# Optimization experiments

Hardware: AMD Instinct MI355X
Metric: run time of the kernel (lower is better)

The kernel has to match this reference:

```python
import jax, jax.numpy as jnp
import numpy as np

NUM_CHUNKS = 8
N = 8192            # points per chunk
STRIDE = 6144
TOTAL = STRIDE * (NUM_CHUNKS - 1) + N  # 51200
OVERLAP_RATIO = 0.3


def setup_inputs() -> dict:
    key = jax.random.key(0)
    ks = jax.random.split(key, 14)
    # Points in a tiny box so all pairwise distances < threshold=0.1 -> full overlap masks.
    chunks = jax.random.uniform(ks[0], (NUM_CHUNKS, N, 3), dtype=jnp.float32) * 0.05
    s = 0.1  # small conv-weight scale keeps smoothed outputs within the threshold box
    return {
        "chunks": chunks,
        "bs_w1": jax.random.normal(ks[1], (32, 3, 5), jnp.float32) * s,
        "bs_b1": jax.random.normal(ks[2], (32,), jnp.float32) * s,
        "bs_w2": jax.random.normal(ks[3], (32, 32, 5), jnp.float32) * s,
        "bs_b2": jax.random.normal(ks[4], (32,), jnp.float32) * s,
        "bs_w3": jax.random.normal(ks[5], (3, 32, 5), jnp.float32) * s,
        "bs_b3": jax.random.normal(ks[6], (3,), jnp.float32) * s,
        "wp_w1": jax.random.normal(ks[7], (32, 6, 1), jnp.float32) * s,
        "wp_b1": jax.random.normal(ks[8], (32,), jnp.float32) * s,
        "wp_w2": jax.random.normal(ks[9], (16, 32, 1), jnp.float32) * s,
        "wp_b2": jax.random.normal(ks[10], (16,), jnp.float32) * s,
        "wp_w3": jax.random.normal(ks[11], (1, 16, 1), jnp.float32) * s,
        "wp_b3": jax.random.normal(ks[12], (1,), jnp.float32) * s,
    }


def _conv1d(x, w, b, pad):
    # x: [Cin, L], w: [Cout, Cin, K] -> [Cout, L]
    y = jax.lax.conv_general_dilated(x[None], w, (1,), [(pad, pad)],
                                     dimension_numbers=("NCH", "OIH", "NCH"))[0]
    return y + b[:, None]


def reference(chunks, bs_w1, bs_b1, bs_w2, bs_b2, bs_w3, bs_b3,
              wp_w1, wp_b1, wp_w2, wp_b2, wp_w3, wp_b3):
    def boundary_smoother(x):   # x: [3, L] -> [3, L]
        h = jax.nn.relu(_conv1d(x, bs_w1, bs_b1, 2))
        h = jax.nn.relu(_conv1d(h, bs_w2, bs_b2, 2))
        return _conv1d(h, bs_w3, bs_b3, 2)

    def weight_predictor(x):    # x: [6, L] -> [L]
        h = jax.nn.relu(_conv1d(x, wp_w1, wp_b1, 0))
        h = jax.nn.relu(_conv1d(h, wp_w2, wp_b2, 0))
        return jax.nn.sigmoid(_conv1d(h, wp_w3, wp_b3, 0))[0]

    def smooth_pair(p, c):      # p, c: [N, 3]; full overlap (masks all-True by construction)
        # squared cdist via the Gram trick; argmin equals cdist argmin
        d2 = (jnp.sum(p * p, 1)[:, None] + jnp.sum(c * c, 1)[None, :]
              - 2.0 * p @ c.T)                       # [N, N]
        mi = jnp.argmin(d2, axis=1)                  # [N]
        matched = c[mi]                              # [N, 3]
        feat = jnp.concatenate([p.T, matched.T], 0)  # [6, N]
        w = weight_predictor(feat)                   # [N]
        fused = w[:, None] * p + (1.0 - w)[:, None] * matched
        sm = boundary_smoother(fused.T).T            # [N, 3]
        # chunk1 fully overlapped -> replaced; chunk2 scatter-written at matched idx
        return sm, c.at[mi].set(sm)

    smoothed = [chunks[0]]
    for i in range(1, NUM_CHUNKS):
        p_new, c_new = smooth_pair(smoothed[-1], chunks[i])
        smoothed[-1] = p_new
        smoothed.append(c_new)
    stacked = jnp.stack(smoothed)                    # [C, N, 3]

    # fade-weighted scatter-add merge
    fade = int(N * OVERLAP_RATIO / 2)
    cw = jnp.ones(N, jnp.float32)
    cw = cw.at[:fade].set(jnp.linspace(0.1, 1.0, fade, dtype=jnp.float32))
    cw = cw.at[-fade:].set(jnp.linspace(1.0, 0.1, fade, dtype=jnp.float32))
    idx = (np.arange(NUM_CHUNKS)[:, None] * STRIDE + np.arange(N)).reshape(-1)
    merged = jnp.zeros((TOTAL, 3), jnp.float32).at[idx].add(
        (stacked * cw[None, :, None]).reshape(-1, 3))
    wsum = jnp.zeros(TOTAL, jnp.float32).at[idx].add(
        jnp.broadcast_to(cw, (NUM_CHUNKS, N)).reshape(-1))
    return merged / jnp.maximum(wsum, 1e-8)[:, None]
```

## Files before the change

### kernel.cpp

```cpp
#include <hip/hip_runtime.h>

#define NPTS 8192
#define NCH 8
#define STRIDE 6144
#define TOTAL 51200
#define FADE 1228
#define SEG 32
#define SEGLEN 256
#define JB 4
#define TEAMS 4
#define TLEN 64

__global__ void k_setup(const float* __restrict__ chunks, float* __restrict__ fin,
                        int* __restrict__ jmax_all, unsigned int* __restrict__ packed32) {
    int i = blockIdx.x * 256 + threadIdx.x;
    if (i < NCH * NPTS * 3) fin[i] = chunks[i];
    if (i < (NCH - 1) * NPTS) jmax_all[i] = -1;
    if (i < (NCH - 1) * NPTS * 2) packed32[i] = 0xFFFFFFFFu;
}

__global__ __launch_bounds__(1024) void k_argmin(const float* __restrict__ P,
                                                 const float* __restrict__ C,
                                                 unsigned long long* __restrict__ packed) {
#pragma clang fp contract(off)
    __shared__ float4 sh[SEGLEN];
    __shared__ unsigned long long pkbuf[TEAMS - 1][1024];
    int tid = threadIdx.x;
    int lt   = tid & 255;
    int team = tid >> 8;
    int k0 = blockIdx.y * SEGLEN;
    if (tid < SEGLEN) {
        int k = k0 + tid;
        float x = C[k * 3 + 0], y = C[k * 3 + 1], z = C[k * 3 + 2];
        float cc = (x * x + y * y) + z * z;
        sh[tid] = make_float4(x, y, z, cc);
    }
    __syncthreads();
    int j0 = blockIdx.x * (256 * JB) + lt * JB;
    const float4* Pv = (const float4*)(P + j0 * 3);
    float4 a = Pv[0], b = Pv[1], c4 = Pv[2];
    float p0[JB] = {a.x, a.w, b.z, c4.y};
    float p1[JB] = {a.y, b.x, b.w, c4.z};
    float p2[JB] = {a.z, b.y, c4.x, c4.w};
    float pp[JB], best[JB];
    int bt[JB];
    int t0 = team * TLEN;
#pragma unroll
    for (int i = 0; i < JB; ++i) {
        pp[i] = (p0[i] * p0[i] + p1[i] * p1[i]) + p2[i] * p2[i];
        best[i] = 3.4e38f;
        bt[i] = t0;
    }
#pragma unroll 4
    for (int tt = 0; tt < TLEN; ++tt) {
        int t = t0 + tt;
        float4 f = sh[t];
#pragma unroll
        for (int i = 0; i < JB; ++i) {
            float g = __builtin_fmaf(p2[i], f.z, __builtin_fmaf(p1[i], f.y, p0[i] * f.x));
            float sadd = pp[i] + f.w;
            float d = __builtin_fmaf(-2.0f, g, sadd);
            if (d < best[i]) { best[i] = d; bt[i] = t; }
        }
    }
    unsigned long long pk[JB];
#pragma unroll
    for (int i = 0; i < JB; ++i) {
        unsigned ud = __float_as_uint(best[i]);
        if (ud == 0x80000000u) ud = 0u;
        ud = (ud & 0x80000000u) ? ~ud : (ud | 0x80000000u);
        pk[i] = ((unsigned long long)ud << 32)
              | (unsigned long long)(unsigned)(k0 + bt[i]);
    }
    if (team > 0) {
#pragma unroll
        for (int i = 0; i < JB; ++i) pkbuf[team - 1][lt * JB + i] = pk[i];
    }
    __syncthreads();
    if (team == 0) {
#pragma unroll
        for (int i = 0; i < JB; ++i) {
            unsigned long long v = pk[i];
            unsigned long long v1 = pkbuf[0][lt * JB + i];
            unsigned long long v2 = pkbuf[1][lt * JB + i];
            unsigned long long v3 = pkbuf[2][lt * JB + i];
            if (v1 < v) v = v1;
            if (v2 < v) v = v2;
            if (v3 < v) v = v3;
            atomicMin(&packed[j0 + i], v);
        }
    }
}

__global__ __launch_bounds__(128) void k_resolve(
        const float* __restrict__ P, const float* __restrict__ C,
        const unsigned long long* __restrict__ packed,
        const float* __restrict__ w1g, const float* __restrict__ b1g,
        const float* __restrict__ w2g, const float* __restrict__ b2g,
        const float* __restrict__ w3g, const float* __restrict__ b3g,
        float* __restrict__ fused, int* __restrict__ mi, int* __restrict__ jmax) {
#pragma clang fp contract(off)
    __shared__ float W[780];
    int tid = threadIdx.x;
    for (int i = tid; i < 780; i += 128) {
        float v;
        if (i < 192) v = w1g[i];
        else if (i < 224) v = b1g[i - 192];
        else if (i < 736) v = w2g[i - 224];
        else if (i < 752) v = b2g[i - 736];
        else if (i < 768) v = w3g[i - 752];
        else v = b3g[0];
        W[i] = v;
    }
    __syncthreads();

    int j = blockIdx.x * 128 + tid;
    int m = (int)(unsigned)(packed[j] & 0xFFFFFFFFull);
    mi[j] = m;
    float x6[6];
    x6[0] = P[j * 3 + 0]; x6[1] = P[j * 3 + 1]; x6[2] = P[j * 3 + 2];
    x6[3] = C[m * 3 + 0]; x6[4] = C[m * 3 + 1]; x6[5] = C[m * 3 + 2];

    float h1[32];
#pragma unroll
    for (int o = 0; o < 32; ++o) {
        float acc = 0.0f;
#pragma unroll
        for (int ci = 0; ci < 6; ++ci) acc = __builtin_fmaf(x6[ci], W[o * 6 + ci], acc);
        h1[o] = fmaxf(acc + W[192 + o], 0.0f);
    }
    float h2[16];
#pragma unroll
    for (int o = 0; o < 16; ++o) {
        float acc = 0.0f;
#pragma unroll
        for (int ci = 0; ci < 32; ++ci) acc = __builtin_fmaf(h1[ci], W[224 + o * 32 + ci], acc);
        h2[o] = fmaxf(acc + W[736 + o], 0.0f);
    }
    float acc = 0.0f;
#pragma unroll
    for (int ci = 0; ci < 16; ++ci) acc = __builtin_fmaf(h2[ci], W[752 + ci], acc);
    float z = acc + W[768];
    float w = 1.0f / (1.0f + expf(-z));
    float omw = 1.0f - w;
#pragma unroll
    for (int e = 0; e < 3; ++e) {
        float t1 = w * x6[e];
        float t2 = omw * x6[3 + e];
        fused[e * NPTS + j] = t1 + t2;
    }

    int lane = tid & 63;
    bool issue = true;
    for (int s = 1; s < 64; ++s) {
        int om = __shfl_down(m, s);
        if (lane + s < 64 && om == m) issue = false;
    }
    if (issue) atomicMax(&jmax[m], j);
}

#define S1 41
#define S2 37
__global__ __launch_bounds__(256) void k_smoother(const float* __restrict__ fused,
        const float* __restrict__ w1g, const float* __restrict__ b1g,
        const float* __restrict__ w2g, const float* __restrict__ b2g,
        const float* __restrict__ w3g, const float* __restrict__ b3g,
        float* __restrict__ sm, const int* __restrict__ mi,
        const int* __restrict__ jmax, float* __restrict__ finNext) {
#pragma clang fp contract(off)
    __shared__ float F[3][44];
    __shared__ float H1[32][S1];
    __shared__ float H2[32][S2];
    __shared__ float W2[5120];
    __shared__ float B2[32];
    int tid = threadIdx.x;
    int BASE = blockIdx.x * 32;

    for (int li = tid; li < 132; li += 256) {
        int c = li / 44, i = li % 44;
        int t = BASE - 6 + i;
        F[c][i] = (t >= 0 && t < NPTS) ? fused[c * NPTS + t] : 0.0f;
    }
    for (int li = tid; li < 1280; li += 256) {
        float4 v = ((const float4*)w2g)[li];
        int base = li * 4;
#pragma unroll
        for (int u = 0; u < 4; ++u) {
            int idx = base + u;
            int co = idx / 160;
            int r = idx - co * 160;
            int ci = r / 5;
            int k = r - ci * 5;
            W2[(ci * 5 + k) * 32 + co] = (&v.x)[u];
        }
    }
    if (tid < 32) B2[tid] = b2g[tid];
    __syncthreads();

    {
        int co = tid >> 3, pg = tid & 7;
        float wr[15];
#pragma unroll
        for (int q = 0; q < 15; ++q) wr[q] = w1g[co * 15 + q];
        float bias = b1g[co];
#pragma unroll
        for (int s = 0; s < 5; ++s) {
            int i = pg * 5 + s;
            int t = BASE - 4 + i;
            float acc = 0.0f;
#pragma unroll
            for (int k = 0; k < 5; ++k)
#pragma unroll
                for (int ci = 0; ci < 3; ++ci)
                    acc = __builtin_fmaf(F[ci][i + k], wr[ci * 5 + k], acc);
            H1[co][i] = (t >= 0 && t < NPTS) ? fmaxf(acc + bias, 0.0f) : 0.0f;
        }
    }
    __syncthreads();

    {
        int cq = tid & 7, pp = tid >> 3;
        if (pp < 18) {
            int i2 = pp * 2;
            int co0 = cq * 4;
            float acc00 = 0.f, acc01 = 0.f, acc02 = 0.f, acc03 = 0.f;
            float acc10 = 0.f, acc11 = 0.f, acc12 = 0.f, acc13 = 0.f;
            for (int k = 0; k < 5; ++k) {
#pragma unroll
                for (int ci = 0; ci < 32; ++ci) {
                    float in0 = H1[ci][i2 + k];
                    float in1 = H1[ci][i2 + k + 1];
                    const float4 wv = *(const float4*)&W2[(ci * 5 + k) * 32 + co0];
                    acc00 = __builtin_fmaf(in0, wv.x, acc00);
                    acc01 = __builtin_fmaf(in0, wv.y, acc01);
                    acc02 = __builtin_fmaf(in0, wv.z, acc02);
                    acc03 = __builtin_fmaf(in0, wv.w, acc03);
                    acc10 = __builtin_fmaf(in1, wv.x, acc10);
                    acc11 = __builtin_fmaf(in1, wv.y, acc11);
                    acc12 = __builtin_fmaf(in1, wv.z, acc12);
                    acc13 = __builtin_fmaf(in1, wv.w, acc13);
                }
            }
            int t0 = BASE - 2 + i2, t1 = t0 + 1;
            bool ok0 = (t0 >= 0 && t0 < NPTS), ok1 = (t1 >= 0 && t1 < NPTS);
            H2[co0 + 0][i2]     = ok0 ? fmaxf(acc00 + B2[co0 + 0], 0.0f) : 0.0f;
            H2[co0 + 1][i2]     = ok0 ? fmaxf(acc01 + B2[co0 + 1], 0.0f) : 0.0f;
            H2[co0 + 2][i2]     = ok0 ? fmaxf(acc02 + B2[co0 + 2], 0.0f) : 0.0f;
            H2[co0 + 3][i2]     = ok0 ? fmaxf(acc03 + B2[co0 + 3], 0.0f) : 0.0f;
            H2[co0 + 0][i2 + 1] = ok1 ? fmaxf(acc10 + B2[co0 + 0], 0.0f) : 0.0f;
            H2[co0 + 1][i2 + 1] = ok1 ? fmaxf(acc11 + B2[co0 + 1], 0.0f) : 0.0f;
            H2[co0 + 2][i2 + 1] = ok1 ? fmaxf(acc12 + B2[co0 + 2], 0.0f) : 0.0f;
            H2[co0 + 3][i2 + 1] = ok1 ? fmaxf(acc13 + B2[co0 + 3], 0.0f) : 0.0f;
        }
    }
    __syncthreads();

    if (tid < 96) {
        int co = tid >> 5, p = tid & 31;
        float wr[160];
        const float4* w3v = (const float4*)(w3g + co * 160);
#pragma unroll
        for (int q = 0; q < 40; ++q) {
            float4 v = w3v[q];
            wr[q * 4 + 0] = v.x; wr[q * 4 + 1] = v.y;
            wr[q * 4 + 2] = v.z; wr[q * 4 + 3] = v.w;
        }
        float acc = 0.0f;
#pragma unroll
        for (int k = 0; k < 5; ++k)
#pragma unroll
            for (int ci = 0; ci < 32; ++ci)
                acc = __builtin_fmaf(H2[ci][p + k], wr[ci * 5 + k], acc);
        float val = acc + b3g[co];
        int jj = BASE + p;
        sm[jj * 3 + co] = val;
        int kk = mi[jj];
        if (jmax[kk] == jj) finNext[kk * 3 + co] = val;
    }
}

__global__ void k_merge(const float* __restrict__ fin, float* __restrict__ out) {
#pragma clang fp contract(off)
    int pos = blockIdx.x * 256 + threadIdx.x;
    if (pos >= TOTAL) return;
    int imax = pos / STRIDE; if (imax > NCH - 1) imax = NCH - 1;
    int imin = (pos >= NPTS) ? ((pos - NPTS) / STRIDE + 1) : 0;
    float a0 = 0.0f, a1 = 0.0f, a2 = 0.0f, wsum = 0.0f;
    const float kstep = 0.9f / 1227.0f;
    for (int i = imin; i <= imax; ++i) {
        int t = pos - i * STRIDE;
        float cw;
        if (t < FADE)                cw = 0.1f + (float)t * kstep;
        else if (t >= NPTS - FADE)   cw = 1.0f - (float)(t - (NPTS - FADE)) * kstep;
        else                         cw = 1.0f;
        const float* v = fin + (i * NPTS + t) * 3;
        a0 += cw * v[0];
        a1 += cw * v[1];
        a2 += cw * v[2];
        wsum += cw;
    }
    float wm = fmaxf(wsum, 1e-8f);
    out[pos * 3 + 0] = a0 / wm;
    out[pos * 3 + 1] = a1 / wm;
    out[pos * 3 + 2] = a2 / wm;
}

extern "C" void kernel_launch(void* const* d_in, const int* in_sizes, int n_in,
                              void* d_out, int out_size, void* d_ws, size_t ws_size,
                              hipStream_t stream) {
    const float* chunks = (const float*)d_in[0];
    const float* bs_w1 = (const float*)d_in[1];
    const float* bs_b1 = (const float*)d_in[2];
    const float* bs_w2 = (const float*)d_in[3];
    const float* bs_b2 = (const float*)d_in[4];
    const float* bs_w3 = (const float*)d_in[5];
    const float* bs_b3 = (const float*)d_in[6];
    const float* wp_w1 = (const float*)d_in[7];
    const float* wp_b1 = (const float*)d_in[8];
    const float* wp_w2 = (const float*)d_in[9];
    const float* wp_b2 = (const float*)d_in[10];
    const float* wp_w3 = (const float*)d_in[11];
    const float* wp_b3 = (const float*)d_in[12];

    unsigned long long* packed_all = (unsigned long long*)d_ws;
    float* fin      = (float*)(packed_all + (NCH - 1) * NPTS);
    float* fused    = fin + NCH * NPTS * 3;
    int*   mi       = (int*)(fused + 3 * NPTS);
    int*   jmax_all = mi + NPTS;

    k_setup<<<768, 256, 0, stream>>>(chunks, fin, jmax_all, (unsigned int*)packed_all);

    for (int i = 1; i < NCH; ++i) {
        const float* C = chunks + i * NPTS * 3;
        float* P  = fin + (i - 1) * NPTS * 3;
        float* Pn = fin + i * NPTS * 3;
        unsigned long long* packed = packed_all + (i - 1) * NPTS;
        int* jmax = jmax_all + (i - 1) * NPTS;

        k_argmin<<<dim3(NPTS / (256 * JB), SEG), 1024, 0, stream>>>(P, C, packed);
        k_resolve<<<64, 128, 0, stream>>>(P, C, packed, wp_w1, wp_b1, wp_w2, wp_b2,
                                          wp_w3, wp_b3, fused, mi, jmax);
        k_smoother<<<256, 256, 0, stream>>>(fused, bs_w1, bs_b1, bs_w2, bs_b2,
                                            bs_w3, bs_b3, P, mi, jmax, Pn);
    }

    k_merge<<<200, 256, 0, stream>>>(fin, (float*)d_out);
}
```

Baseline: 328.4 us.

## Fuse all per-chunk kernels into one cooperative persistent kernel with grid syncs

Replaces the setup, 7×(argmin, resolve, smoother), and merge launches with a single cooperative kernel of 256 blocks × 1024 threads that uses grid.sync between phases. Weights are staged into shared memory once and reused across iterations, and the wave-level dedup before atomicMax is dropped. This removes about 23 kernel launches and their gaps. In exchange, the resolve and smoother phases run on only 32–256 threads of each 1024-thread block, and grid-wide barriers add their own cost. The launch also requires all 256 blocks to be co-resident.

```diff
diff --git a/kernel.cpp b/kernel.cpp
--- a/kernel.cpp
+++ b/kernel.cpp
@@ -1,4 +1,7 @@
 #include <hip/hip_runtime.h>
+#include <hip/hip_cooperative_groups.h>
+
+namespace cg = cooperative_groups;
 
 #define NPTS 8192
 #define NCH 8
@@ -10,179 +13,62 @@
 #define JB 4
 #define TEAMS 4
 #define TLEN 64
-
-__global__ void k_setup(const float* __restrict__ chunks, float* __restrict__ fin,
-                        int* __restrict__ jmax_all, unsigned int* __restrict__ packed32) {
-    int i = blockIdx.x * 256 + threadIdx.x;
-    if (i < NCH * NPTS * 3) fin[i] = chunks[i];
-    if (i < (NCH - 1) * NPTS) jmax_all[i] = -1;
-    if (i < (NCH - 1) * NPTS * 2) packed32[i] = 0xFFFFFFFFu;
-}
-
-__global__ __launch_bounds__(1024) void k_argmin(const float* __restrict__ P,
-                                                 const float* __restrict__ C,
-                                                 unsigned long long* __restrict__ packed) {
+#define S1 41
+#define S2 37
+
+__global__ __launch_bounds__(1024, 4) void k_mega(
+        const float* __restrict__ chunks,
+        const float* __restrict__ bs_w1, const float* __restrict__ bs_b1,
+        const float* __restrict__ bs_w2, const float* __restrict__ bs_b2,
+        const float* __restrict__ bs_w3, const float* __restrict__ bs_b3,
+        const float* __restrict__ wp_w1, const float* __restrict__ wp_b1,
+        const float* __restrict__ wp_w2, const float* __restrict__ wp_b2,
+        const float* __restrict__ wp_w3, const float* __restrict__ wp_b3,
+        float* __restrict__ out, unsigned long long* ws) {
 #pragma clang fp contract(off)
+    cg::grid_group grid = cg::this_grid();
+
     __shared__ float4 sh[SEGLEN];
     __shared__ unsigned long long pkbuf[TEAMS - 1][1024];
-    int tid = threadIdx.x;
-    int lt   = tid & 255;
-    int team = tid >> 8;
-    int k0 = blockIdx.y * SEGLEN;
-    if (tid < SEGLEN) {
-        int k = k0 + tid;
-        float x = C[k * 3 + 0], y = C[k * 3 + 1], z = C[k * 3 + 2];
-        float cc = (x * x + y * y) + z * z;
-        sh[tid] = make_float4(x, y, z, cc);
-    }
-    __syncthreads();
-    int j0 = blockIdx.x * (256 * JB) + lt * JB;
-    const float4* Pv = (const float4*)(P + j0 * 3);
-    float4 a = Pv[0], b = Pv[1], c4 = Pv[2];
-    float p0[JB] = {a.x, a.w, b.z, c4.y};
-    float p1[JB] = {a.y, b.x, b.w, c4.z};
-    float p2[JB] = {a.z, b.y, c4.x, c4.w};
-    float pp[JB], best[JB];
-    int bt[JB];
-    int t0 = team * TLEN;
-#pragma unroll
-    for (int i = 0; i < JB; ++i) {
-        pp[i] = (p0[i] * p0[i] + p1[i] * p1[i]) + p2[i] * p2[i];
-        best[i] = 3.4e38f;
-        bt[i] = t0;
-    }
-#pragma unroll 4
-    for (int tt = 0; tt < TLEN; ++tt) {
-        int t = t0 + tt;
-        float4 f = sh[t];
-#pragma unroll
-        for (int i = 0; i < JB; ++i) {
-            float g = __builtin_fmaf(p2[i], f.z, __builtin_fmaf(p1[i], f.y, p0[i] * f.x));
-            float sadd = pp[i] + f.w;
-            float d = __builtin_fmaf(-2.0f, g, sadd);
-            if (d < best[i]) { best[i] = d; bt[i] = t; }
-        }
-    }
-    unsigned long long pk[JB];
-#pragma unroll
-    for (int i = 0; i < JB; ++i) {
-        unsigned ud = __float_as_uint(best[i]);
-        if (ud == 0x80000000u) ud = 0u;
-        ud = (ud & 0x80000000u) ? ~ud : (ud | 0x80000000u);
-        pk[i] = ((unsigned long long)ud << 32)
-              | (unsigned long long)(unsigned)(k0 + bt[i]);
-    }
-    if (team > 0) {
-#pragma unroll
-        for (int i = 0; i < JB; ++i) pkbuf[team - 1][lt * JB + i] = pk[i];
-    }
-    __syncthreads();
-    if (team == 0) {
-#pragma unroll
-        for (int i = 0; i < JB; ++i) {
-            unsigned long long v = pk[i];
-            unsigned long long v1 = pkbuf[0][lt * JB + i];
-            unsigned long long v2 = pkbuf[1][lt * JB + i];
-            unsigned long long v3 = pkbuf[2][lt * JB + i];
-            if (v1 < v) v = v1;
-            if (v2 < v) v = v2;
-            if (v3 < v) v = v3;
-            atomicMin(&packed[j0 + i], v);
-        }
-    }
-}
-
-__global__ __launch_bounds__(128) void k_resolve(
-        const float* __restrict__ P, const float* __restrict__ C,
-        const unsigned long long* __restrict__ packed,
-        const float* __restrict__ w1g, const float* __restrict__ b1g,
-        const float* __restrict__ w2g, const float* __restrict__ b2g,
-        const float* __restrict__ w3g, const float* __restrict__ b3g,
-        float* __restrict__ fused, int* __restrict__ mi, int* __restrict__ jmax) {
-#pragma clang fp contract(off)
-    __shared__ float W[780];
-    int tid = threadIdx.x;
-    for (int i = tid; i < 780; i += 128) {
-        float v;
-        if (i < 192) v = w1g[i];
-        else if (i < 224) v = b1g[i - 192];
-        else if (i < 736) v = w2g[i - 224];
-        else if (i < 752) v = b2g[i - 736];
-        else if (i < 768) v = w3g[i - 752];
-        else v = b3g[0];
-        W[i] = v;
-    }
-    __syncthreads();
-
-    int j = blockIdx.x * 128 + tid;
-    int m = (int)(unsigned)(packed[j] & 0xFFFFFFFFull);
-    mi[j] = m;
-    float x6[6];
-    x6[0] = P[j * 3 + 0]; x6[1] = P[j * 3 + 1]; x6[2] = P[j * 3 + 2];
-    x6[3] = C[m * 3 + 0]; x6[4] = C[m * 3 + 1]; x6[5] = C[m * 3 + 2];
-
-    float h1[32];
-#pragma unroll
-    for (int o = 0; o < 32; ++o) {
-        float acc = 0.0f;
-#pragma unroll
-        for (int ci = 0; ci < 6; ++ci) acc = __builtin_fmaf(x6[ci], W[o * 6 + ci], acc);
-        h1[o] = fmaxf(acc + W[192 + o], 0.0f);
-    }
-    float h2[16];
-#pragma unroll
-    for (int o = 0; o < 16; ++o) {
-        float acc = 0.0f;
-#pragma unroll
-        for (int ci = 0; ci < 32; ++ci) acc = __builtin_fmaf(h1[ci], W[224 + o * 32 + ci], acc);
-        h2[o] = fmaxf(acc + W[736 + o], 0.0f);
-    }
-    float acc = 0.0f;
-#pragma unroll
-    for (int ci = 0; ci < 16; ++ci) acc = __builtin_fmaf(h2[ci], W[752 + ci], acc);
-    float z = acc + W[768];
-    float w = 1.0f / (1.0f + expf(-z));
-    float omw = 1.0f - w;
-#pragma unroll
-    for (int e = 0; e < 3; ++e) {
-        float t1 = w * x6[e];
-        float t2 = omw * x6[3 + e];
-        fused[e * NPTS + j] = t1 + t2;
-    }
-
-    int lane = tid & 63;
-    bool issue = true;
-    for (int s = 1; s < 64; ++s) {
-        int om = __shfl_down(m, s);
-        if (lane + s < 64 && om == m) issue = false;
-    }
-    if (issue) atomicMax(&jmax[m], j);
-}
-
-#define S1 41
-#define S2 37
-__global__ __launch_bounds__(256) void k_smoother(const float* __restrict__ fused,
-        const float* __restrict__ w1g, const float* __restrict__ b1g,
-        const float* __restrict__ w2g, const float* __restrict__ b2g,
-        const float* __restrict__ w3g, const float* __restrict__ b3g,
-        float* __restrict__ sm, const int* __restrict__ mi,
-        const int* __restrict__ jmax, float* __restrict__ finNext) {
-#pragma clang fp contract(off)
+    __shared__ float Wp[780];
     __shared__ float F[3][44];
     __shared__ float H1[32][S1];
     __shared__ float H2[32][S2];
+    __shared__ float W1s[480];
+    __shared__ float B1s[32];
     __shared__ float W2[5120];
     __shared__ float B2[32];
+    __shared__ float W3s[480];
+    __shared__ float B3s[3];
+
+    unsigned long long* packed_all = ws;
+    float* fin      = (float*)(packed_all + (NCH - 1) * NPTS);
+    float* fused    = fin + NCH * NPTS * 3;
+    int*   mi       = (int*)(fused + 3 * NPTS);
+    int*   jmax_all = mi + NPTS;
+
     int tid = threadIdx.x;
-    int BASE = blockIdx.x * 32;
-
-    for (int li = tid; li < 132; li += 256) {
-        int c = li / 44, i = li % 44;
-        int t = BASE - 6 + i;
-        F[c][i] = (t >= 0 && t < NPTS) ? fused[c * NPTS + t] : 0.0f;
-    }
-    for (int li = tid; li < 1280; li += 256) {
-        float4 v = ((const float4*)w2g)[li];
+    int bid = blockIdx.x;
+    int gtid = bid * 1024 + tid;
+
+    if (gtid < NCH * NPTS * 3) fin[gtid] = chunks[gtid];
+    if (gtid < (NCH - 1) * NPTS) {
+        jmax_all[gtid] = -1;
+        packed_all[gtid] = 0xFFFFFFFFFFFFFFFFull;
+    }
+
+    for (int i = tid; i < 780; i += 1024) {
+        float v;
+        if (i < 192) v = wp_w1[i];
+        else if (i < 224) v = wp_b1[i - 192];
+        else if (i < 736) v = wp_w2[i - 224];
+        else if (i < 752) v = wp_b2[i - 736];
+        else if (i < 768) v = wp_w3[i - 752];
+        else v = wp_b3[0];
+        Wp[i] = v;
+    }
+    for (int li = tid; li < 1280; li += 1024) {
+        float4 v = ((const float4*)bs_w2)[li];
         int base = li * 4;
 #pragma unroll
         for (int u = 0; u < 4; ++u) {
@@ -194,115 +80,235 @@
             W2[(ci * 5 + k) * 32 + co] = (&v.x)[u];
         }
     }
-    if (tid < 32) B2[tid] = b2g[tid];
-    __syncthreads();
-
-    {
-        int co = tid >> 3, pg = tid & 7;
-        float wr[15];
-#pragma unroll
-        for (int q = 0; q < 15; ++q) wr[q] = w1g[co * 15 + q];
-        float bias = b1g[co];
-#pragma unroll
-        for (int s = 0; s < 5; ++s) {
-            int i = pg * 5 + s;
-            int t = BASE - 4 + i;
+    for (int i = tid; i < 480; i += 1024) { W1s[i] = bs_w1[i]; W3s[i] = bs_w3[i]; }
+    if (tid < 32) { B1s[tid] = bs_b1[tid]; B2[tid] = bs_b2[tid]; }
+    if (tid < 3)  B3s[tid] = bs_b3[tid];
+
+    grid.sync();
+
+    for (int it = 1; it < NCH; ++it) {
+        const float* C = chunks + it * NPTS * 3;
+        float* P  = fin + (it - 1) * NPTS * 3;
+        float* Pn = fin + it * NPTS * 3;
+        unsigned long long* packed = packed_all + (it - 1) * NPTS;
+        int* jmax = jmax_all + (it - 1) * NPTS;
+
+        {
+            int bx = bid & 7, by = bid >> 3;
+            int lt = tid & 255, team = tid >> 8;
+            int k0 = by * SEGLEN;
+            if (tid < SEGLEN) {
+                int k = k0 + tid;
+                float x = C[k * 3 + 0], y = C[k * 3 + 1], z = C[k * 3 + 2];
+                float cc = (x * x + y * y) + z * z;
+                sh[tid] = make_float4(x, y, z, cc);
+            }
+            __syncthreads();
+            int j0 = bx * (256 * JB) + lt * JB;
+            const float4* Pv = (const float4*)(P + j0 * 3);
+            float4 a = Pv[0], b = Pv[1], c4 = Pv[2];
+            float p0[JB] = {a.x, a.w, b.z, c4.y};
+            float p1[JB] = {a.y, b.x, b.w, c4.z};
+            float p2[JB] = {a.z, b.y, c4.x, c4.w};
+            float pp[JB], best[JB];
+            int bt[JB];
+            int t0 = team * TLEN;
+#pragma unroll
+            for (int i = 0; i < JB; ++i) {
+                pp[i] = (p0[i] * p0[i] + p1[i] * p1[i]) + p2[i] * p2[i];
+                best[i] = 3.4e38f;
+                bt[i] = t0;
+            }
+#pragma unroll 4
+            for (int tt = 0; tt < TLEN; ++tt) {
+                int t = t0 + tt;
+                float4 f = sh[t];
+#pragma unroll
+                for (int i = 0; i < JB; ++i) {
+                    float g = __builtin_fmaf(p2[i], f.z, __builtin_fmaf(p1[i], f.y, p0[i] * f.x));
+                    float sadd = pp[i] + f.w;
+                    float d = __builtin_fmaf(-2.0f, g, sadd);
+                    if (d < best[i]) { best[i] = d; bt[i] = t; }
+                }
+            }
+            unsigned long long pk[JB];
+#pragma unroll
+            for (int i = 0; i < JB; ++i) {
+                unsigned ud = __float_as_uint(best[i]);
+                if (ud == 0x80000000u) ud = 0u;
+                ud = (ud & 0x80000000u) ? ~ud : (ud | 0x80000000u);
+                pk[i] = ((unsigned long long)ud << 32)
+                      | (unsigned long long)(unsigned)(k0 + bt[i]);
+            }
+            if (team > 0) {
+#pragma unroll
+                for (int i = 0; i < JB; ++i) pkbuf[team - 1][lt * JB + i] = pk[i];
+            }
+            __syncthreads();
+            if (team == 0) {
+#pragma unroll
+                for (int i = 0; i < JB; ++i) {
+                    unsigned long long v = pk[i];
+                    unsigned long long v1 = pkbuf[0][lt * JB + i];
+                    unsigned long long v2 = pkbuf[1][lt * JB + i];
+                    unsigned long long v3 = pkbuf[2][lt * JB + i];
+                    if (v1 < v) v = v1;
+                    if (v2 < v) v = v2;
+                    if (v3 < v) v = v3;
+                    atomicMin(&packed[j0 + i], v);
+                }
+            }
+        }
+        grid.sync();
+
+        if (tid < 32) {
+            int j = bid * 32 + tid;
+            int m = (int)(unsigned)(packed[j] & 0xFFFFFFFFull);
+            mi[j] = m;
+            float x6[6];
+            x6[0] = P[j * 3 + 0]; x6[1] = P[j * 3 + 1]; x6[2] = P[j * 3 + 2];
+            x6[3] = C[m * 3 + 0]; x6[4] = C[m * 3 + 1]; x6[5] = C[m * 3 + 2];
+
+            float h1[32];
+#pragma unroll
+            for (int o = 0; o < 32; ++o) {
+                float acc = 0.0f;
+#pragma unroll
+                for (int ci = 0; ci < 6; ++ci) acc = __builtin_fmaf(x6[ci], Wp[o * 6 + ci], acc);
+                h1[o] = fmaxf(acc + Wp[192 + o], 0.0f);
+            }
+            float h2[16];
+#pragma unroll
+            for (int o = 0; o < 16; ++o) {
+                float acc = 0.0f;
+#pragma unroll
+                for (int ci = 0; ci < 32; ++ci) acc = __builtin_fmaf(h1[ci], Wp[224 + o * 32 + ci], acc);
+                h2[o] = fmaxf(acc + Wp[736 + o], 0.0f);
+            }
             float acc = 0.0f;
 #pragma unroll
-            for (int k = 0; k < 5; ++k)
-#pragma unroll
-                for (int ci = 0; ci < 3; ++ci)
-                    acc = __builtin_fmaf(F[ci][i + k], wr[ci * 5 + k], acc);
-            H1[co][i] = (t >= 0 && t < NPTS) ? fmaxf(acc + bias, 0.0f) : 0.0f;
-        }
-    }
-    __syncthreads();
-
-    {
-        int cq = tid & 7, pp = tid >> 3;
-        if (pp < 18) {
-            int i2 = pp * 2;
-            int co0 = cq * 4;
-            float acc00 = 0.f, acc01 = 0.f, acc02 = 0.f, acc03 = 0.f;
-            float acc10 = 0.f, acc11 = 0.f, acc12 = 0.f, acc13 = 0.f;
-            for (int k = 0; k < 5; ++k) {
-#pragma unroll
-                for (int ci = 0; ci < 32; ++ci) {
-                    float in0 = H1[ci][i2 + k];
-                    float in1 = H1[ci][i2 + k + 1];
-                    const float4 wv = *(const float4*)&W2[(ci * 5 + k) * 32 + co0];
-                    acc00 = __builtin_fmaf(in0, wv.x, acc00);
-                    acc01 = __builtin_fmaf(in0, wv.y, acc01);
-                    acc02 = __builtin_fmaf(in0, wv.z, acc02);
-                    acc03 = __builtin_fmaf(in0, wv.w, acc03);
-                    acc10 = __builtin_fmaf(in1, wv.x, acc10);
-                    acc11 = __builtin_fmaf(in1, wv.y, acc11);
-                    acc12 = __builtin_fmaf(in1, wv.z, acc12);
-                    acc13 = __builtin_fmaf(in1, wv.w, acc13);
+            for (int ci = 0; ci < 16; ++ci) acc = __builtin_fmaf(h2[ci], Wp[752 + ci], acc);
+            float z = acc + Wp[768];
+            float w = 1.0f / (1.0f + expf(-z));
+            float omw = 1.0f - w;
+#pragma unroll
+            for (int e = 0; e < 3; ++e) {
+                float t1 = w * x6[e];
+                float t2 = omw * x6[3 + e];
+                fused[e * NPTS + j] = t1 + t2;
+            }
+            atomicMax(&jmax[m], j);
+        }
+        grid.sync();
+
+        {
+            int BASE = bid * 32;
+            for (int li = tid; li < 132; li += 1024) {
+                int c = li / 44, i = li % 44;
+                int t = BASE - 6 + i;
+                F[c][i] = (t >= 0 && t < NPTS) ? fused[c * NPTS + t] : 0.0f;
+            }
+            __syncthreads();
+
+            if (tid < 256) {
+                int co = tid >> 3, pg = tid & 7;
+                float wr[15];
+#pragma unroll
+                for (int q = 0; q < 15; ++q) wr[q] = W1s[co * 15 + q];
+                float bias = B1s[co];
+#pragma unroll
+                for (int s = 0; s < 5; ++s) {
+                    int i = pg * 5 + s;
+                    int t = BASE - 4 + i;
+                    float acc = 0.0f;
+#pragma unroll
+                    for (int k = 0; k < 5; ++k)
+#pragma unroll
+                        for (int ci = 0; ci < 3; ++ci)
+                            acc = __builtin_fmaf(F[ci][i + k], wr[ci * 5 + k], acc);
+                    H1[co][i] = (t >= 0 && t < NPTS) ? fmaxf(acc + bias, 0.0f) : 0.0f;
                 }
             }
-            int t0 = BASE - 2 + i2, t1 = t0 + 1;
-            bool ok0 = (t0 >= 0 && t0 < NPTS), ok1 = (t1 >= 0 && t1 < NPTS);
-            H2[co0 + 0][i2]     = ok0 ? fmaxf(acc00 + B2[co0 + 0], 0.0f) : 0.0f;
-            H2[co0 + 1][i2]     = ok0 ? fmaxf(acc01 + B2[co0 + 1], 0.0f) : 0.0f;
-            H2[co0 + 2][i2]     = ok0 ? fmaxf(acc02 + B2[co0 + 2], 0.0f) : 0.0f;
-            H2[co0 + 3][i2]     = ok0 ? fmaxf(acc03 + B2[co0 + 3], 0.0f) : 0.0f;
-            H2[co0 + 0][i2 + 1] = ok1 ? fmaxf(acc10 + B2[co0 + 0], 0.0f) : 0.0f;
-            H2[co0 + 1][i2 + 1] = ok1 ? fmaxf(acc11 + B2[co0 + 1], 0.0f) : 0.0f;
-            H2[co0 + 2][i2 + 1] = ok1 ? fmaxf(acc12 + B2[co0 + 2], 0.0f) : 0.0f;
-            H2[co0 + 3][i2 + 1] = ok1 ? fmaxf(acc13 + B2[co0 + 3], 0.0f) : 0.0f;
-        }
-    }
-    __syncthreads();
-
-    if (tid < 96) {
-        int co = tid >> 5, p = tid & 31;
-        float wr[160];
-        const float4* w3v = (const float4*)(w3g + co * 160);
-#pragma unroll
-        for (int q = 0; q < 40; ++q) {
-            float4 v = w3v[q];
-            wr[q * 4 + 0] = v.x; wr[q * 4 + 1] = v.y;
-            wr[q * 4 + 2] = v.z; wr[q * 4 + 3] = v.w;
-        }
-        float acc = 0.0f;
-#pragma unroll
-        for (int k = 0; k < 5; ++k)
-#pragma unroll
-            for (int ci = 0; ci < 32; ++ci)
-                acc = __builtin_fmaf(H2[ci][p + k], wr[ci * 5 + k], acc);
-        float val = acc + b3g[co];
-        int jj = BASE + p;
-        sm[jj * 3 + co] = val;
-        int kk = mi[jj];
-        if (jmax[kk] == jj) finNext[kk * 3 + co] = val;
-    }
-}
-
-__global__ void k_merge(const float* __restrict__ fin, float* __restrict__ out) {
-#pragma clang fp contract(off)
-    int pos = blockIdx.x * 256 + threadIdx.x;
-    if (pos >= TOTAL) return;
-    int imax = pos / STRIDE; if (imax > NCH - 1) imax = NCH - 1;
-    int imin = (pos >= NPTS) ? ((pos - NPTS) / STRIDE + 1) : 0;
-    float a0 = 0.0f, a1 = 0.0f, a2 = 0.0f, wsum = 0.0f;
-    const float kstep = 0.9f / 1227.0f;
-    for (int i = imin; i <= imax; ++i) {
-        int t = pos - i * STRIDE;
-        float cw;
-        if (t < FADE)                cw = 0.1f + (float)t * kstep;
-        else if (t >= NPTS - FADE)   cw = 1.0f - (float)(t - (NPTS - FADE)) * kstep;
-        else                         cw = 1.0f;
-        const float* v = fin + (i * NPTS + t) * 3;
-        a0 += cw * v[0];
-        a1 += cw * v[1];
-        a2 += cw * v[2];
-        wsum += cw;
-    }
-    float wm = fmaxf(wsum, 1e-8f);
-    out[pos * 3 + 0] = a0 / wm;
-    out[pos * 3 + 1] = a1 / wm;
-    out[pos * 3 + 2] = a2 / wm;
+            __syncthreads();
+
+            {
+                int cq = tid & 7, pq = tid >> 3;
+                if (pq < 18) {
+                    int i2 = pq * 2;
+                    int co0 = cq * 4;
+                    float acc00 = 0.f, acc01 = 0.f, acc02 = 0.f, acc03 = 0.f;
+                    float acc10 = 0.f, acc11 = 0.f, acc12 = 0.f, acc13 = 0.f;
+                    for (int k = 0; k < 5; ++k) {
+#pragma unroll
+                        for (int ci = 0; ci < 32; ++ci) {
+                            float in0 = H1[ci][i2 + k];
+                            float in1 = H1[ci][i2 + k + 1];
+                            const float4 wv = *(const float4*)&W2[(ci * 5 + k) * 32 + co0];
+                            acc00 = __builtin_fmaf(in0, wv.x, acc00);
+                            acc01 = __builtin_fmaf(in0, wv.y, acc01);
+                            acc02 = __builtin_fmaf(in0, wv.z, acc02);
+                            acc03 = __builtin_fmaf(in0, wv.w, acc03);
+                            acc10 = __builtin_fmaf(in1, wv.x, acc10);
+                            acc11 = __builtin_fmaf(in1, wv.y, acc11);
+                            acc12 = __builtin_fmaf(in1, wv.z, acc12);
+                            acc13 = __builtin_fmaf(in1, wv.w, acc13);
+                        }
+                    }
+                    int t0 = BASE - 2 + i2, t1 = t0 + 1;
+                    bool ok0 = (t0 >= 0 && t0 < NPTS), ok1 = (t1 >= 0 && t1 < NPTS);
+                    H2[co0 + 0][i2]     = ok0 ? fmaxf(acc00 + B2[co0 + 0], 0.0f) : 0.0f;
+                    H2[co0 + 1][i2]     = ok0 ? fmaxf(acc01 + B2[co0 + 1], 0.0f) : 0.0f;
+                    H2[co0 + 2][i2]     = ok0 ? fmaxf(acc02 + B2[co0 + 2], 0.0f) : 0.0f;
+                    H2[co0 + 3][i2]     = ok0 ? fmaxf(acc03 + B2[co0 + 3], 0.0f) : 0.0f;
+                    H2[co0 + 0][i2 + 1] = ok1 ? fmaxf(acc10 + B2[co0 + 0], 0.0f) : 0.0f;
+                    H2[co0 + 1][i2 + 1] = ok1 ? fmaxf(acc11 + B2[co0 + 1], 0.0f) : 0.0f;
+                    H2[co0 + 2][i2 + 1] = ok1 ? fmaxf(acc12 + B2[co0 + 2], 0.0f) : 0.0f;
+                    H2[co0 + 3][i2 + 1] = ok1 ? fmaxf(acc13 + B2[co0 + 3], 0.0f) : 0.0f;
+                }
+            }
+            __syncthreads();
+
+            if (tid < 96) {
+                int co = tid >> 5, p = tid & 31;
+                float acc = 0.0f;
+#pragma unroll
+                for (int k = 0; k < 5; ++k)
+#pragma unroll
+                    for (int ci = 0; ci < 32; ++ci)
+                        acc = __builtin_fmaf(H2[ci][p + k], W3s[co * 160 + ci * 5 + k], acc);
+                float val = acc + B3s[co];
+                int jj = BASE + p;
+                P[jj * 3 + co] = val;
+                int kk = mi[jj];
+                if (jmax[kk] == jj) Pn[kk * 3 + co] = val;
+            }
+        }
+        grid.sync();
+    }
+
+    if (gtid < TOTAL) {
+        int pos = gtid;
+        int imax = pos / STRIDE; if (imax > NCH - 1) imax = NCH - 1;
+        int imin = (pos >= NPTS) ? ((pos - NPTS) / STRIDE + 1) : 0;
+        float a0 = 0.0f, a1 = 0.0f, a2 = 0.0f, wsum = 0.0f;
+        const float kstep = 0.9f / 1227.0f;
+        for (int i = imin; i <= imax; ++i) {
+            int t = pos - i * STRIDE;
+            float cw;
+            if (t < FADE)                cw = 0.1f + (float)t * kstep;
+            else if (t >= NPTS - FADE)   cw = 1.0f - (float)(t - (NPTS - FADE)) * kstep;
+            else                         cw = 1.0f;
+            const float* v = fin + (i * NPTS + t) * 3;
+            a0 += cw * v[0];
+            a1 += cw * v[1];
+            a2 += cw * v[2];
+            wsum += cw;
+        }
+        float wm = fmaxf(wsum, 1e-8f);
+        out[pos * 3 + 0] = a0 / wm;
+        out[pos * 3 + 1] = a1 / wm;
+        out[pos * 3 + 2] = a2 / wm;
+    }
 }
 
 extern "C" void kernel_launch(void* const* d_in, const int* in_sizes, int n_in,
@@ -321,28 +327,16 @@
     const float* wp_b2 = (const float*)d_in[10];
     const float* wp_w3 = (const float*)d_in[11];
     const float* wp_b3 = (const float*)d_in[12];
-
-    unsigned long long* packed_all = (unsigned long long*)d_ws;
-    float* fin      = (float*)(packed_all + (NCH - 1) * NPTS);
-    float* fused    = fin + NCH * NPTS * 3;
-    int*   mi       = (int*)(fused + 3 * NPTS);
-    int*   jmax_all = mi + NPTS;
-
-    k_setup<<<768, 256, 0, stream>>>(chunks, fin, jmax_all, (unsigned int*)packed_all);
-
-    for (int i = 1; i < NCH; ++i) {
-        const float* C = chunks + i * NPTS * 3;
-        float* P  = fin + (i - 1) * NPTS * 3;
-        float* Pn = fin + i * NPTS * 3;
-        unsigned long long* packed = packed_all + (i - 1) * NPTS;
-        int* jmax = jmax_all + (i - 1) * NPTS;
-
-        k_argmin<<<dim3(NPTS / (256 * JB), SEG), 1024, 0, stream>>>(P, C, packed);
-        k_resolve<<<64, 128, 0, stream>>>(P, C, packed, wp_w1, wp_b1, wp_w2, wp_b2,
-                                          wp_w3, wp_b3, fused, mi, jmax);
-        k_smoother<<<256, 256, 0, stream>>>(fused, bs_w1, bs_b1, bs_w2, bs_b2,
-                                            bs_w3, bs_b3, P, mi, jmax, Pn);
-    }
-
-    k_merge<<<200, 256, 0, stream>>>(fin, (float*)d_out);
+    float* outp = (float*)d_out;
+    unsigned long long* wsp = (unsigned long long*)d_ws;
+
+    void* args[] = {
+        (void*)&chunks,
+        (void*)&bs_w1, (void*)&bs_b1, (void*)&bs_w2, (void*)&bs_b2,
+        (void*)&bs_w3, (void*)&bs_b3,
+        (void*)&wp_w1, (void*)&wp_b1, (void*)&wp_w2, (void*)&wp_b2,
+        (void*)&wp_w3, (void*)&wp_b3,
+        (void*)&outp, (void*)&wsp};
+    hipLaunchCooperativeKernel((const void*)k_mega, dim3(256), dim3(1024),
+                               args, 0, stream);
 }
```

After: 1.017 ms. 210% more time.

## Fuse resolve into smoother and replace jmax pass with packed 64-bit atomicMax scatter

Applied to the files above, without the earlier changes.

Merges the weight-predictor kernel into the smoother kernel, so each block computes its own fused inputs (a 32-point tile plus a 12-point halo) in shared memory. This removes one launch per chunk pair and the global round trip of the fused, mi and jmax arrays. The last-writer scatter rule is now a single 64-bit atomicMax that packs (index+1, value) into 64-bit point storage, which replaces the separate jmax resolution. In exchange, halo points are recomputed redundantly and point loads in argmin and merge become 64-bit reads at twice the bandwidth. Only 44 threads per block run the MLP, which serializes that phase.

```diff
diff --git a/kernel.cpp b/kernel.cpp
--- a/kernel.cpp
+++ b/kernel.cpp
@@ -10,21 +10,24 @@
 #define JB 4
 #define TEAMS 4
 #define TLEN 64
-
-__global__ void k_setup(const float* __restrict__ chunks, float* __restrict__ fin,
-                        int* __restrict__ jmax_all, unsigned int* __restrict__ packed32) {
+#define S1 41
+#define S2 37
+
+typedef unsigned long long u64;
+
+__global__ void k_setup(const float* __restrict__ chunks, u64* __restrict__ PK,
+                        u64* __restrict__ packed_all) {
     int i = blockIdx.x * 256 + threadIdx.x;
-    if (i < NCH * NPTS * 3) fin[i] = chunks[i];
-    if (i < (NCH - 1) * NPTS) jmax_all[i] = -1;
-    if (i < (NCH - 1) * NPTS * 2) packed32[i] = 0xFFFFFFFFu;
-}
-
-__global__ __launch_bounds__(1024) void k_argmin(const float* __restrict__ P,
+    if (i < NCH * NPTS * 3) PK[i] = (u64)__float_as_uint(chunks[i]);
+    if (i < (NCH - 1) * NPTS) packed_all[i] = 0xFFFFFFFFFFFFFFFFull;
+}
+
+__global__ __launch_bounds__(1024) void k_argmin(const u64* __restrict__ PKprev,
                                                  const float* __restrict__ C,
-                                                 unsigned long long* __restrict__ packed) {
+                                                 u64* __restrict__ packed) {
 #pragma clang fp contract(off)
     __shared__ float4 sh[SEGLEN];
-    __shared__ unsigned long long pkbuf[TEAMS - 1][1024];
+    __shared__ u64 pkbuf[TEAMS - 1][1024];
     int tid = threadIdx.x;
     int lt   = tid & 255;
     int team = tid >> 8;
@@ -37,11 +40,13 @@
     }
     __syncthreads();
     int j0 = blockIdx.x * (256 * JB) + lt * JB;
-    const float4* Pv = (const float4*)(P + j0 * 3);
-    float4 a = Pv[0], b = Pv[1], c4 = Pv[2];
-    float p0[JB] = {a.x, a.w, b.z, c4.y};
-    float p1[JB] = {a.y, b.x, b.w, c4.z};
-    float p2[JB] = {a.z, b.y, c4.x, c4.w};
+    const u64* Pq = PKprev + (size_t)j0 * 3;
+    float p[12];
+#pragma unroll
+    for (int n = 0; n < 12; ++n) p[n] = __uint_as_float((unsigned)Pq[n]);
+    float p0[JB] = {p[0], p[3], p[6], p[9]};
+    float p1[JB] = {p[1], p[4], p[7], p[10]};
+    float p2[JB] = {p[2], p[5], p[8], p[11]};
     float pp[JB], best[JB];
     int bt[JB];
     int t0 = team * TLEN;
@@ -63,14 +68,13 @@
             if (d < best[i]) { best[i] = d; bt[i] = t; }
         }
     }
-    unsigned long long pk[JB];
+    u64 pk[JB];
 #pragma unroll
     for (int i = 0; i < JB; ++i) {
         unsigned ud = __float_as_uint(best[i]);
         if (ud == 0x80000000u) ud = 0u;
         ud = (ud & 0x80000000u) ? ~ud : (ud | 0x80000000u);
-        pk[i] = ((unsigned long long)ud << 32)
-              | (unsigned long long)(unsigned)(k0 + bt[i]);
+        pk[i] = ((u64)ud << 32) | (u64)(unsigned)(k0 + bt[i]);
     }
     if (team > 0) {
 #pragma unroll
@@ -80,10 +84,10 @@
     if (team == 0) {
 #pragma unroll
         for (int i = 0; i < JB; ++i) {
-            unsigned long long v = pk[i];
-            unsigned long long v1 = pkbuf[0][lt * JB + i];
-            unsigned long long v2 = pkbuf[1][lt * JB + i];
-            unsigned long long v3 = pkbuf[2][lt * JB + i];
+            u64 v = pk[i];
+            u64 v1 = pkbuf[0][lt * JB + i];
+            u64 v2 = pkbuf[1][lt * JB + i];
+            u64 v3 = pkbuf[2][lt * JB + i];
             if (v1 < v) v = v1;
             if (v2 < v) v = v2;
             if (v3 < v) v = v3;
@@ -92,83 +96,20 @@
     }
 }
 
-__global__ __launch_bounds__(128) void k_resolve(
-        const float* __restrict__ P, const float* __restrict__ C,
-        const unsigned long long* __restrict__ packed,
+__global__ __launch_bounds__(256) void k_rsm(
+        const u64* __restrict__ PKprev, const float* __restrict__ C,
+        const u64* __restrict__ packed,
+        const float* __restrict__ wp_w1, const float* __restrict__ wp_b1,
+        const float* __restrict__ wp_w2, const float* __restrict__ wp_b2,
+        const float* __restrict__ wp_w3, const float* __restrict__ wp_b3,
         const float* __restrict__ w1g, const float* __restrict__ b1g,
         const float* __restrict__ w2g, const float* __restrict__ b2g,
         const float* __restrict__ w3g, const float* __restrict__ b3g,
-        float* __restrict__ fused, int* __restrict__ mi, int* __restrict__ jmax) {
+        float* __restrict__ finOut, u64* __restrict__ PKnext) {
 #pragma clang fp contract(off)
-    __shared__ float W[780];
-    int tid = threadIdx.x;
-    for (int i = tid; i < 780; i += 128) {
-        float v;
-        if (i < 192) v = w1g[i];
-        else if (i < 224) v = b1g[i - 192];
-        else if (i < 736) v = w2g[i - 224];
-        else if (i < 752) v = b2g[i - 736];
-        else if (i < 768) v = w3g[i - 752];
-        else v = b3g[0];
-        W[i] = v;
-    }
-    __syncthreads();
-
-    int j = blockIdx.x * 128 + tid;
-    int m = (int)(unsigned)(packed[j] & 0xFFFFFFFFull);
-    mi[j] = m;
-    float x6[6];
-    x6[0] = P[j * 3 + 0]; x6[1] = P[j * 3 + 1]; x6[2] = P[j * 3 + 2];
-    x6[3] = C[m * 3 + 0]; x6[4] = C[m * 3 + 1]; x6[5] = C[m * 3 + 2];
-
-    float h1[32];
-#pragma unroll
-    for (int o = 0; o < 32; ++o) {
-        float acc = 0.0f;
-#pragma unroll
-        for (int ci = 0; ci < 6; ++ci) acc = __builtin_fmaf(x6[ci], W[o * 6 + ci], acc);
-        h1[o] = fmaxf(acc + W[192 + o], 0.0f);
-    }
-    float h2[16];
-#pragma unroll
-    for (int o = 0; o < 16; ++o) {
-        float acc = 0.0f;
-#pragma unroll
-        for (int ci = 0; ci < 32; ++ci) acc = __builtin_fmaf(h1[ci], W[224 + o * 32 + ci], acc);
-        h2[o] = fmaxf(acc + W[736 + o], 0.0f);
-    }
-    float acc = 0.0f;
-#pragma unroll
-    for (int ci = 0; ci < 16; ++ci) acc = __builtin_fmaf(h2[ci], W[752 + ci], acc);
-    float z = acc + W[768];
-    float w = 1.0f / (1.0f + expf(-z));
-    float omw = 1.0f - w;
-#pragma unroll
-    for (int e = 0; e < 3; ++e) {
-        float t1 = w * x6[e];
-        float t2 = omw * x6[3 + e];
-        fused[e * NPTS + j] = t1 + t2;
-    }
-
-    int lane = tid & 63;
-    bool issue = true;
-    for (int s = 1; s < 64; ++s) {
-        int om = __shfl_down(m, s);
-        if (lane + s < 64 && om == m) issue = false;
-    }
-    if (issue) atomicMax(&jmax[m], j);
-}
-
-#define S1 41
-#define S2 37
-__global__ __launch_bounds__(256) void k_smoother(const float* __restrict__ fused,
-        const float* __restrict__ w1g, const float* __restrict__ b1g,
-        const float* __restrict__ w2g, const float* __restrict__ b2g,
-        const float* __restrict__ w3g, const float* __restrict__ b3g,
-        float* __restrict__ sm, const int* __restrict__ mi,
-        const int* __restrict__ jmax, float* __restrict__ finNext) {
-#pragma clang fp contract(off)
+    __shared__ float Wp[780];
     __shared__ float F[3][44];
+    __shared__ int   MIs[44];
     __shared__ float H1[32][S1];
     __shared__ float H2[32][S2];
     __shared__ float W2[5120];
@@ -176,10 +117,15 @@
     int tid = threadIdx.x;
     int BASE = blockIdx.x * 32;
 
-    for (int li = tid; li < 132; li += 256) {
-        int c = li / 44, i = li % 44;
-        int t = BASE - 6 + i;
-        F[c][i] = (t >= 0 && t < NPTS) ? fused[c * NPTS + t] : 0.0f;
+    for (int i = tid; i < 780; i += 256) {
+        float v;
+        if (i < 192) v = wp_w1[i];
+        else if (i < 224) v = wp_b1[i - 192];
+        else if (i < 736) v = wp_w2[i - 224];
+        else if (i < 752) v = wp_b2[i - 736];
+        else if (i < 768) v = wp_w3[i - 752];
+        else v = wp_b3[0];
+        Wp[i] = v;
     }
     for (int li = tid; li < 1280; li += 256) {
         float4 v = ((const float4*)w2g)[li];
@@ -197,6 +143,52 @@
     if (tid < 32) B2[tid] = b2g[tid];
     __syncthreads();
 
+    if (tid < 44) {
+        int jt = BASE - 6 + tid;
+        if (jt >= 0 && jt < NPTS) {
+            int m = (int)(unsigned)(packed[jt] & 0xFFFFFFFFull);
+            MIs[tid] = m;
+            float x6[6];
+            x6[0] = __uint_as_float((unsigned)PKprev[(size_t)jt * 3 + 0]);
+            x6[1] = __uint_as_float((unsigned)PKprev[(size_t)jt * 3 + 1]);
+            x6[2] = __uint_as_float((unsigned)PKprev[(size_t)jt * 3 + 2]);
+            x6[3] = C[m * 3 + 0]; x6[4] = C[m * 3 + 1]; x6[5] = C[m * 3 + 2];
+
+            float h1[32];
+#pragma unroll
+            for (int o = 0; o < 32; ++o) {
+                float acc = 0.0f;
+#pragma unroll
+                for (int ci = 0; ci < 6; ++ci) acc = __builtin_fmaf(x6[ci], Wp[o * 6 + ci], acc);
+                h1[o] = fmaxf(acc + Wp[192 + o], 0.0f);
+            }
+            float h2[16];
+#pragma unroll
+            for (int o = 0; o < 16; ++o) {
+                float acc = 0.0f;
+#pragma unroll
+                for (int ci = 0; ci < 32; ++ci) acc = __builtin_fmaf(h1[ci], Wp[224 + o * 32 + ci], acc);
+                h2[o] = fmaxf(acc + Wp[736 + o], 0.0f);
+            }
+            float acc = 0.0f;
+#pragma unroll
+            for (int ci = 0; ci < 16; ++ci) acc = __builtin_fmaf(h2[ci], Wp[752 + ci], acc);
+            float z = acc + Wp[768];
+            float w = 1.0f / (1.0f + expf(-z));
+            float omw = 1.0f - w;
+#pragma unroll
+            for (int e = 0; e < 3; ++e) {
+                float t1 = w * x6[e];
+                float t2 = omw * x6[3 + e];
+                F[e][tid] = t1 + t2;
+            }
+        } else {
+            F[0][tid] = 0.0f; F[1][tid] = 0.0f; F[2][tid] = 0.0f;
+            MIs[tid] = 0;
+        }
+    }
+    __syncthreads();
+
     {
         int co = tid >> 3, pg = tid & 7;
         float wr[15];
@@ -219,9 +211,9 @@
     __syncthreads();
 
     {
-        int cq = tid & 7, pp = tid >> 3;
-        if (pp < 18) {
-            int i2 = pp * 2;
+        int cq = tid & 7, pq = tid >> 3;
+        if (pq < 18) {
+            int i2 = pq * 2;
             int co0 = cq * 4;
             float acc00 = 0.f, acc01 = 0.f, acc02 = 0.f, acc03 = 0.f;
             float acc10 = 0.f, acc11 = 0.f, acc12 = 0.f, acc13 = 0.f;
@@ -273,13 +265,15 @@
                 acc = __builtin_fmaf(H2[ci][p + k], wr[ci * 5 + k], acc);
         float val = acc + b3g[co];
         int jj = BASE + p;
-        sm[jj * 3 + co] = val;
-        int kk = mi[jj];
-        if (jmax[kk] == jj) finNext[kk * 3 + co] = val;
-    }
-}
-
-__global__ void k_merge(const float* __restrict__ fin, float* __restrict__ out) {
+        finOut[jj * 3 + co] = val;
+        int kk = MIs[p + 6];
+        atomicMax(&PKnext[(size_t)kk * 3 + co],
+                  ((u64)(unsigned)(jj + 1) << 32) | (u64)__float_as_uint(val));
+    }
+}
+
+__global__ void k_merge(const float* __restrict__ fin, const u64* __restrict__ PK7,
+                        float* __restrict__ out) {
 #pragma clang fp contract(off)
     int pos = blockIdx.x * 256 + threadIdx.x;
     if (pos >= TOTAL) return;
@@ -293,10 +287,19 @@
         if (t < FADE)                cw = 0.1f + (float)t * kstep;
         else if (t >= NPTS - FADE)   cw = 1.0f - (float)(t - (NPTS - FADE)) * kstep;
         else                         cw = 1.0f;
-        const float* v = fin + (i * NPTS + t) * 3;
-        a0 += cw * v[0];
-        a1 += cw * v[1];
-        a2 += cw * v[2];
+        float v0, v1, v2;
+        if (i < NCH - 1) {
+            const float* v = fin + ((size_t)i * NPTS + t) * 3;
+            v0 = v[0]; v1 = v[1]; v2 = v[2];
+        } else {
+            const u64* q = PK7 + (size_t)t * 3;
+            v0 = __uint_as_float((unsigned)q[0]);
+            v1 = __uint_as_float((unsigned)q[1]);
+            v2 = __uint_as_float((unsigned)q[2]);
+        }
+        a0 += cw * v0;
+        a1 += cw * v1;
+        a2 += cw * v2;
         wsum += cw;
     }
     float wm = fmaxf(wsum, 1e-8f);
@@ -322,27 +325,25 @@
     const float* wp_w3 = (const float*)d_in[11];
     const float* wp_b3 = (const float*)d_in[12];
 
-    unsigned long long* packed_all = (unsigned long long*)d_ws;
-    float* fin      = (float*)(packed_all + (NCH - 1) * NPTS);
-    float* fused    = fin + NCH * NPTS * 3;
-    int*   mi       = (int*)(fused + 3 * NPTS);
-    int*   jmax_all = mi + NPTS;
-
-    k_setup<<<768, 256, 0, stream>>>(chunks, fin, jmax_all, (unsigned int*)packed_all);
-
-    for (int i = 1; i < NCH; ++i) {
-        const float* C = chunks + i * NPTS * 3;
-        float* P  = fin + (i - 1) * NPTS * 3;
-        float* Pn = fin + i * NPTS * 3;
-        unsigned long long* packed = packed_all + (i - 1) * NPTS;
-        int* jmax = jmax_all + (i - 1) * NPTS;
-
-        k_argmin<<<dim3(NPTS / (256 * JB), SEG), 1024, 0, stream>>>(P, C, packed);
-        k_resolve<<<64, 128, 0, stream>>>(P, C, packed, wp_w1, wp_b1, wp_w2, wp_b2,
-                                          wp_w3, wp_b3, fused, mi, jmax);
-        k_smoother<<<256, 256, 0, stream>>>(fused, bs_w1, bs_b1, bs_w2, bs_b2,
-                                            bs_w3, bs_b3, P, mi, jmax, Pn);
-    }
-
-    k_merge<<<200, 256, 0, stream>>>(fin, (float*)d_out);
-}
+    u64* packed_all = (u64*)d_ws;
+    u64* PK         = packed_all + (NCH - 1) * NPTS;
+    float* fin      = (float*)(PK + NCH * NPTS * 3);
+
+    k_setup<<<768, 256, 0, stream>>>(chunks, PK, packed_all);
+
+    for (int it = 1; it < NCH; ++it) {
+        const float* C = chunks + it * NPTS * 3;
+        const u64* PKprev = PK + (size_t)(it - 1) * NPTS * 3;
+        u64* PKnext = PK + (size_t)it * NPTS * 3;
+        u64* packed = packed_all + (it - 1) * NPTS;
+        float* finOut = fin + (size_t)(it - 1) * NPTS * 3;
+
+        k_argmin<<<dim3(NPTS / (256 * JB), SEG), 1024, 0, stream>>>(PKprev, C, packed);
+        k_rsm<<<256, 256, 0, stream>>>(PKprev, C, packed,
+                                       wp_w1, wp_b1, wp_w2, wp_b2, wp_w3, wp_b3,
+                                       bs_w1, bs_b1, bs_w2, bs_b2, bs_w3, bs_b3,
+                                       finOut, PKnext);
+    }
+
+    k_merge<<<200, 256, 0, stream>>>(fin, PK + (size_t)(NCH - 1) * NPTS * 3, (float*)d_out);
+}
```

After: 667.2 us. +103.2%, slower.
